# Optimization experiments

Hardware: AMD Instinct MI355X
Metric: run time of the kernel (lower is better)

## Reference

```python
import jax, jax.numpy as jnp
import numpy as np

R, F, E, P = 32768, 64, 16, 10

def setup_inputs() -> dict:
    key = jax.random.key(0)
    k1, k2 = jax.random.split(key)
    x = jax.random.normal(k1, (R, F, E), dtype=jnp.float32)
    # xavier-uniform-like init for weights (P, F)
    bound = float(np.sqrt(6.0 / (P + F)))
    weights = jax.random.uniform(k2, (P, F), dtype=jnp.float32, minval=-bound, maxval=bound)
    return {"x": x, "weights": weights}

def reference(x, weights):
    # delta[r,p,f,e] = x[r,f,e] * w[p,f]; lp[r,p] = sum_{f,e} delta^2
    # = sum_f w[p,f]^2 * sum_e x[r,f,e]^2  (exact algebraic identity,
    # avoids the O(R*P*F*E) intermediate the torch code materializes)
    x_sq = jnp.sum(x * x, axis=-1)            # [R, F]
    w_sq = weights * weights                  # [P, F]
    lp = jnp.einsum('rf,pf->rp', x_sq, w_sq)  # [R, P]
    return lp
```

## Files before the change

### kernel.cpp

```cpp
#include <hip/hip_runtime.h>

constexpr int F = 64;
constexpr int E = 16;
constexpr int P = 10;

__global__ __launch_bounds__(256, 8) void ip_kernel(const float* __restrict__ x,
                                                    const float* __restrict__ w,
                                                    float* __restrict__ out,
                                                    int rows) {
    const int lane = threadIdx.x & 63;
    const int wave_in_block = threadIdx.x >> 6;
    const int waves_per_block = blockDim.x >> 6;
    const int wave_id = blockIdx.x * waves_per_block + wave_in_block;
    const int n_waves = gridDim.x * waves_per_block;

    const int q = lane & 3;
    const int g = lane >> 2;

    float wsq[3][4];
#pragma unroll
    for (int j = 0; j < 3; ++j) {
        const int p = q + 4 * j;
#pragma unroll
        for (int seg = 0; seg < 4; ++seg) {
            const float wv = (p < P) ? w[p * F + seg * 16 + g] : 0.0f;
            wsq[j][seg] = wv * wv;
        }
    }

    for (int r = wave_id; r < rows; r += n_waves) {
        const float4* xrow = (const float4*)(x + (size_t)r * (F * E));
        float4 v[4];
#pragma unroll
        for (int seg = 0; seg < 4; ++seg)
            v[seg] = xrow[seg * 64 + lane];

        float acc0 = 0.0f, acc1 = 0.0f, acc2 = 0.0f;
#pragma unroll
        for (int seg = 0; seg < 4; ++seg) {
            const float4 t = v[seg];
            float sq = t.x * t.x + t.y * t.y + t.z * t.z + t.w * t.w;
            sq += __shfl_xor(sq, 1);
            sq += __shfl_xor(sq, 2);
            acc0 += wsq[0][seg] * sq;
            acc1 += wsq[1][seg] * sq;
            acc2 += wsq[2][seg] * sq;
        }
#pragma unroll
        for (int m = 4; m <= 32; m <<= 1) {
            acc0 += __shfl_xor(acc0, m);
            acc1 += __shfl_xor(acc1, m);
            acc2 += __shfl_xor(acc2, m);
        }
        if (g == 0) {
            float* o = out + (size_t)r * P + q;
            o[0] = acc0;
            o[4] = acc1;
            if (q < 2) o[8] = acc2;
        }
    }
}

extern "C" void kernel_launch(void* const* d_in, const int* in_sizes, int n_in,
                              void* d_out, int out_size, void* d_ws, size_t ws_size,
                              hipStream_t stream) {
    const float* x = (const float*)d_in[0];
    const float* w = (const float*)d_in[1];
    float* out = (float*)d_out;
    const int rows = in_sizes[0] / (F * E);

    dim3 grid(2048), block(256);
    hipLaunchKernelGGL(ip_kernel, grid, block, 0, stream, x, w, out, rows);
}
```

Before: 185.8 us.

## Tile rows per block with LDS staging of squared sums and weights

Each block now processes 16-row tiles. Every thread loads one (row, feature) group of 16 contiguous floats, reduces it to a sum of squares, and stores it in shared memory. A subset of threads then computes the 10 output dot products from shared x-squares and squared weights. This replaces the cross-lane shuffle reductions and raises per-thread loads in flight, at the cost of lane-strided access patterns, block barriers, and idle threads in the output phase.

```diff
diff --git a/kernel.cpp b/kernel.cpp
--- a/kernel.cpp
+++ b/kernel.cpp
@@ -3,61 +3,61 @@
 constexpr int F = 64;
 constexpr int E = 16;
 constexpr int P = 10;
+constexpr int TILE_ROWS = 16;
+constexpr int LDS_PITCH = 68;
 
-__global__ __launch_bounds__(256, 8) void ip_kernel(const float* __restrict__ x,
+__global__ __launch_bounds__(256, 4) void ip_kernel(const float* __restrict__ x,
                                                     const float* __restrict__ w,
                                                     float* __restrict__ out,
-                                                    int rows) {
-    const int lane = threadIdx.x & 63;
-    const int wave_in_block = threadIdx.x >> 6;
-    const int waves_per_block = blockDim.x >> 6;
-    const int wave_id = blockIdx.x * waves_per_block + wave_in_block;
-    const int n_waves = gridDim.x * waves_per_block;
+                                                    int n_tiles) {
+    __shared__ float xsq_s[TILE_ROWS][LDS_PITCH];
+    __shared__ float wsq_s[P][LDS_PITCH];
 
-    const int q = lane & 3;
-    const int g = lane >> 2;
+    const int tid = threadIdx.x;
+    const int f = tid & 63;
+    const int r0 = tid >> 6;
 
-    float wsq[3][4];
-#pragma unroll
-    for (int j = 0; j < 3; ++j) {
-        const int p = q + 4 * j;
-#pragma unroll
-        for (int seg = 0; seg < 4; ++seg) {
-            const float wv = (p < P) ? w[p * F + seg * 16 + g] : 0.0f;
-            wsq[j][seg] = wv * wv;
-        }
+    for (int idx = tid; idx < P * F; idx += 256) {
+        const float wv = w[idx];
+        wsq_s[idx >> 6][idx & 63] = wv * wv;
     }
 
-    for (int r = wave_id; r < rows; r += n_waves) {
-        const float4* xrow = (const float4*)(x + (size_t)r * (F * E));
-        float4 v[4];
+    for (int tile = blockIdx.x; tile < n_tiles; tile += gridDim.x) {
+        const float* xt = x + (size_t)tile * (TILE_ROWS * F * E);
+
+        float4 v[4][4];
 #pragma unroll
-        for (int seg = 0; seg < 4; ++seg)
-            v[seg] = xrow[seg * 64 + lane];
-
-        float acc0 = 0.0f, acc1 = 0.0f, acc2 = 0.0f;
+        for (int k = 0; k < 4; ++k) {
+            const int r = r0 + 4 * k;
+            const float4* src = (const float4*)(xt + ((size_t)r * F + f) * E);
 #pragma unroll
-        for (int seg = 0; seg < 4; ++seg) {
-            const float4 t = v[seg];
-            float sq = t.x * t.x + t.y * t.y + t.z * t.z + t.w * t.w;
-            sq += __shfl_xor(sq, 1);
-            sq += __shfl_xor(sq, 2);
-            acc0 += wsq[0][seg] * sq;
-            acc1 += wsq[1][seg] * sq;
-            acc2 += wsq[2][seg] * sq;
+            for (int s = 0; s < 4; ++s) v[k][s] = src[s];
         }
 #pragma unroll
-        for (int m = 4; m <= 32; m <<= 1) {
-            acc0 += __shfl_xor(acc0, m);
-            acc1 += __shfl_xor(acc1, m);
-            acc2 += __shfl_xor(acc2, m);
+        for (int k = 0; k < 4; ++k) {
+            float s = 0.0f;
+#pragma unroll
+            for (int seg = 0; seg < 4; ++seg) {
+                const float4 t = v[k][seg];
+                s += t.x * t.x + t.y * t.y + t.z * t.z + t.w * t.w;
+            }
+            xsq_s[r0 + 4 * k][f] = s;
         }
-        if (g == 0) {
-            float* o = out + (size_t)r * P + q;
-            o[0] = acc0;
-            o[4] = acc1;
-            if (q < 2) o[8] = acc2;
+        __syncthreads();
+
+        if (tid < TILE_ROWS * P) {
+            const int r = tid / P;
+            const int p = tid % P;
+            float acc = 0.0f;
+#pragma unroll
+            for (int f4 = 0; f4 < F; f4 += 4) {
+                const float4 xa = *(const float4*)&xsq_s[r][f4];
+                const float4 wa = *(const float4*)&wsq_s[p][f4];
+                acc += xa.x * wa.x + xa.y * wa.y + xa.z * wa.z + xa.w * wa.w;
+            }
+            out[(size_t)tile * (TILE_ROWS * P) + tid] = acc;
         }
+        __syncthreads();
     }
 }
 
@@ -68,7 +68,8 @@
     const float* w = (const float*)d_in[1];
     float* out = (float*)d_out;
     const int rows = in_sizes[0] / (F * E);
+    const int n_tiles = rows / TILE_ROWS;
 
     dim3 grid(2048), block(256);
-    hipLaunchKernelGGL(ip_kernel, grid, block, 0, stream, x, w, out, rows);
+    hipLaunchKernelGGL(ip_kernel, grid, block, 0, stream, x, w, out, n_tiles);
 }
```

New measurement: 190.1 us. 1.02x slower.
